# Kernel optimization log

Hardware: AMD Instinct MI355X
Metric: run time of the kernel (lower is better)

Reference implementation:

```python
import jax, jax.numpy as jnp
import numpy as np

EPS = 1e-6
BN_EPS = 1e-5
STAGES = 10


def setup_inputs() -> dict:
    key = jax.random.key(0)
    ks = jax.random.split(key, 8)
    B, L, C, K, INNER = 16, 2048, 256, 64, 4096
    x = jax.random.normal(ks[0], (B, L, C), jnp.float32)
    group_tokens = jax.random.normal(ks[1], (B, K, C), jnp.float32)
    mu0 = jax.random.normal(ks[2], (1, K, C), jnp.float32) * np.sqrt(2.0 / C)
    mu0 = mu0 / (EPS + jnp.linalg.norm(mu0, axis=2, keepdims=True))
    w1 = jax.random.normal(ks[3], (INNER, C), jnp.float32) * 0.02
    b1 = jnp.zeros((INNER,), jnp.float32)
    gamma = jnp.ones((INNER,), jnp.float32)
    beta = jnp.zeros((INNER,), jnp.float32)
    bn_mean = jnp.zeros((INNER,), jnp.float32)
    bn_var = jnp.ones((INNER,), jnp.float32)
    w2 = jax.random.normal(ks[4], (C, INNER), jnp.float32) * 0.02
    b2 = jnp.zeros((C,), jnp.float32)
    return {"x": x, "group_tokens": group_tokens, "mu0": mu0, "w1": w1,
            "b1": b1, "gamma": gamma, "beta": beta, "bn_mean": bn_mean,
            "bn_var": bn_var, "w2": w2, "b2": b2}


def _em_loop(x, mu):
    # x: [B,L,C], mu: [B,K,C]; 10-step soft-clustering fixed point (no_grad in torch)
    def step(carry, _):
        mu, _ = carry
        z = jax.nn.softmax(jnp.einsum('blc,bkc->blk', x, mu), axis=-1)  # [B,L,K]
        z = z / (EPS + z.sum(axis=1, keepdims=True))
        mu = jnp.einsum('blk,blc->bkc', z, x)
        mu = mu / (EPS + jnp.linalg.norm(mu, axis=2, keepdims=True))
        return (mu, z), None
    z0 = jnp.zeros(x.shape[:2] + (mu.shape[1],), x.dtype)
    (mu, z), _ = jax.lax.scan(step, (mu, z0), None, length=STAGES)
    return jax.lax.stop_gradient(mu), jax.lax.stop_gradient(z)


def _project_mlp(x, w1, b1, gamma, beta, bn_mean, bn_var, w2, b2):
    # Conv1d(k=1) == channelwise linear; BN in eval mode with running stats
    h = jnp.einsum('blc,ic->bli', x, w1) + b1                 # [B,L,INNER]
    h = (h - bn_mean) * (gamma / jnp.sqrt(bn_var + BN_EPS)) + beta
    h = jax.nn.relu(h)
    return jnp.einsum('bli,oi->blo', h, w2) + b2              # [B,L,C]


def reference(x, group_tokens, mu0, w1, b1, gamma, beta, bn_mean, bn_var, w2, b2):
    B = group_tokens.shape[0]
    mu = jnp.broadcast_to(mu0, (B,) + mu0.shape[1:])
    mu, z = _em_loop(x, mu)
    recon_x = jnp.einsum('blk,bkc->blc', z, mu)
    recon_x = _project_mlp(recon_x, w1, b1, gamma, beta, bn_mean, bn_var, w2, b2)
    new_z = jax.nn.softmax(jnp.einsum('blc,bkc->blk', x, mu), axis=-1)
    attn_map = new_z / (EPS + new_z.sum(axis=1, keepdims=True))  # [B,L,K]
    attn_map = jnp.transpose(attn_map, (0, 2, 1))[:, None]       # [B,1,K,L]
    return mu, attn_map, recon_x
```

## Files before the change

kernel.cpp:

```cpp
#include <hip/hip_runtime.h>

constexpr int B_ = 16, L_ = 2048, C_ = 256, K_ = 64, INNER_ = 4096;
constexpr int NCH = 16;
constexpr int RPB = 128;
#define EPSF 1e-6f

typedef __attribute__((ext_vector_type(8)))  short bf16x8;
typedef __attribute__((ext_vector_type(4)))  float f32x4;
typedef __attribute__((ext_vector_type(16))) float f32x16;
typedef _Float16 f16;
typedef __attribute__((ext_vector_type(8))) _Float16 f16x8;
typedef __attribute__((ext_vector_type(4))) _Float16 f16x4;

__device__ __forceinline__ unsigned short f2bf(float f) {
  union { float f; unsigned u; } v; v.f = f;
  unsigned r = v.u + 0x7fffu + ((v.u >> 16) & 1u);
  return (unsigned short)(r >> 16);
}

__device__ __forceinline__ void gload16(const void* src, void* lds) {
  __builtin_amdgcn_global_load_lds(
      (const __attribute__((address_space(1))) unsigned*)src,
      (__attribute__((address_space(3))) unsigned*)lds, 16, 0, 0);
}

__global__ __launch_bounds__(256) void k_prext(
    const float* __restrict__ x,
    const float* __restrict__ w1, const float* __restrict__ w2,
    const float* __restrict__ gamma, const float* __restrict__ beta,
    const float* __restrict__ bmean, const float* __restrict__ bvar,
    const float* __restrict__ b1, const float* __restrict__ mu0,
    unsigned short* __restrict__ w1fr, unsigned short* __restrict__ w2fr,
    f16* __restrict__ bnshH, f16* __restrict__ muF,
    f16* __restrict__ xf, f16* __restrict__ xTf)
{
  __shared__ float ts[64][65];
  int bid = blockIdx.x, t = threadIdx.x;
  if (bid < 4096) {
    int i = bid * 256 + t;
    if (i < INNER_ * C_) {
      int j = i & 7, l31 = (i >> 3) & 31;
      {
        int l5 = (i >> 8) & 1, ks = (i >> 9) & 15, ih = (i >> 13) & 1, ic = i >> 14;
        int r1 = ic * 64 + ih * 32 + l31;
        int c1 = ks * 16 + 4 * l5 + 8 * (j >> 2) + (j & 3);
        float sc = gamma[r1] * rsqrtf(bvar[r1] + 1e-5f);
        w1fr[i] = f2bf(w1[(size_t)r1 * C_ + c1] * sc);
      }
      {
        int ot = (i >> 8) & 7, l5 = (i >> 11) & 1, g = i >> 12;
        int o = ot * 32 + l31;
        int ii = g * 16 + 4 * l5 + 8 * (j >> 2) + (j & 3);
        w2fr[i] = f2bf(w2[(size_t)o * INNER_ + ii]);
      }
    }
    if (i < B_ * K_ * C_) muF[i] = (f16)mu0[i & (K_ * C_ - 1)];
    if (i < INNER_) {
      float sc = gamma[i] * rsqrtf(bvar[i] + 1e-5f);
      bnshH[i] = (f16)fmaf(b1[i] - bmean[i], sc, beta[i]);
    }
  } else {
    int b2 = bid - 4096;
    int l0 = (b2 & 31) * 64, c0 = ((b2 >> 5) & 3) * 64, b = b2 >> 7;
    for (int p = 0; p < 16; ++p) {
      int e = t + p * 256, i = e >> 6, j = e & 63;
      float vv = x[((size_t)b * L_ + l0 + i) * C_ + c0 + j];
      ts[i][j] = vv;
      xf[((size_t)b * L_ + l0 + i) * C_ + c0 + j] = (f16)vv;
    }
    __syncthreads();
    for (int p = 0; p < 16; ++p) {
      int e = t + p * 256, i = e >> 6, j = e & 63;
      xTf[((size_t)b * C_ + c0 + i) * L_ + l0 + j] = (f16)ts[j][i];
    }
  }
}

template<bool DO_MU, bool WRITE_Z>
__global__ __launch_bounds__(512, 2) void k_em(
    const f16* __restrict__ xf,
    const f16* __restrict__ xTf,
    const f16* __restrict__ muF,
    f16* __restrict__ zout,
    float* __restrict__ cp,
    f16* __restrict__ part)
{
  __shared__ f16 mu_s[K_ * C_];
  __shared__ f16 zT_s[K_ * RPB];
  __shared__ f16 xtile[C_ * RPB];
  __shared__ float cpart[8][K_];

  int t = threadIdx.x, b = blockIdx.y, chn = blockIdx.x, l0 = chn * RPB;
  int w = t >> 6, lane = t & 63, l15 = lane & 15, g = lane >> 4;

#pragma unroll
  for (int q = 0; q < 4; ++q) {
    int s = q * 512 + t, k = s >> 5, sl = s & 31;
    gload16(muF + (size_t)b * (K_ * C_) + k * C_ + ((sl ^ (k & 15)) << 3), mu_s + s * 8);
  }
  __builtin_amdgcn_sched_barrier(0);
  f16x8 xfr[8];
  const f16* xr = xf + ((size_t)b * L_ + l0 + w * 16 + l15) * C_ + g * 8;
#pragma unroll
  for (int ck = 0; ck < 8; ++ck) xfr[ck] = *(const f16x8*)(xr + ck * 32);
  __builtin_amdgcn_sched_barrier(0);
  if (DO_MU) {
#pragma unroll
    for (int q = 0; q < 8; ++q) {
      int s = q * 512 + t, c = s >> 4, sl = s & 15;
      gload16(xTf + (size_t)(b * C_ + c) * L_ + l0 + ((sl ^ (c & 7)) << 3), xtile + s * 8);
    }
    __builtin_amdgcn_sched_barrier(0);
    asm volatile("s_waitcnt vmcnt(16)" ::: "memory");
  } else {
    asm volatile("s_waitcnt vmcnt(8)" ::: "memory");
  }
  __builtin_amdgcn_s_barrier();
  __builtin_amdgcn_sched_barrier(0);

  f32x4 acc[4];
#pragma unroll
  for (int mt = 0; mt < 4; ++mt)
#pragma unroll
    for (int j = 0; j < 4; ++j) acc[mt][j] = 0.f;
#pragma unroll
  for (int ck = 0; ck < 8; ++ck) {
#pragma unroll
    for (int mt = 0; mt < 4; ++mt) {
      f16x8 a = *(const f16x8*)(mu_s + (mt * 16 + l15) * C_ + (((ck * 4 + g) ^ l15) << 3));
      acc[mt] = __builtin_amdgcn_mfma_f32_16x16x32_f16(a, xfr[ck], acc[mt], 0, 0, 0);
    }
  }

  float z[4][4];
  {
    float mx = acc[0][0];
#pragma unroll
    for (int mt = 0; mt < 4; ++mt)
#pragma unroll
      for (int jj = 0; jj < 4; ++jj) mx = fmaxf(mx, acc[mt][jj]);
    mx = fmaxf(mx, __shfl_xor(mx, 16, 64));
    mx = fmaxf(mx, __shfl_xor(mx, 32, 64));
    float sm = 0.f;
#pragma unroll
    for (int mt = 0; mt < 4; ++mt)
#pragma unroll
      for (int jj = 0; jj < 4; ++jj) {
        float e = __expf(acc[mt][jj] - mx);
        z[mt][jj] = e; sm += e;
      }
    sm += __shfl_xor(sm, 16, 64);
    sm += __shfl_xor(sm, 32, 64);
    float inv = 1.f / sm;
#pragma unroll
    for (int mt = 0; mt < 4; ++mt)
#pragma unroll
      for (int jj = 0; jj < 4; ++jj) z[mt][jj] *= inv;
  }

#pragma unroll
  for (int mt = 0; mt < 4; ++mt)
#pragma unroll
    for (int jj = 0; jj < 4; ++jj) {
      float v = z[mt][jj];
      v += __shfl_xor(v, 1, 64); v += __shfl_xor(v, 2, 64);
      v += __shfl_xor(v, 4, 64); v += __shfl_xor(v, 8, 64);
      if (l15 == 0) cpart[w][mt * 16 + g * 4 + jj] = v;
    }

#pragma unroll
  for (int mt = 0; mt < 4; ++mt)
#pragma unroll
    for (int jj = 0; jj < 4; ++jj) {
      int k = mt * 16 + g * 4 + jj;
      int tl = w * 16 + l15;
      f16 h = (f16)z[mt][jj];
      if (DO_MU)   zT_s[k * RPB + (((tl >> 3) ^ (k & 15)) << 3) + (tl & 7)] = h;
      if (WRITE_Z) zout[((size_t)b * L_ + l0 + tl) * K_ + k] = h;
    }
  __syncthreads();

  if (t < K_) {
    float s = 0.f;
#pragma unroll
    for (int q = 0; q < 8; ++q) s += cpart[q][t];
    cp[(size_t)chn * (B_ * K_) + b * K_ + t] = s;
  }

  if (DO_MU) {
    f32x4 a3[4][2];
#pragma unroll
    for (int mt = 0; mt < 4; ++mt)
#pragma unroll
      for (int nt = 0; nt < 2; ++nt)
#pragma unroll
        for (int j = 0; j < 4; ++j) a3[mt][nt][j] = 0.f;
    int cb = w * 32;
#pragma unroll
    for (int ks = 0; ks < 4; ++ks) {
      f16x8 az[4], bx[2];
#pragma unroll
      for (int mt = 0; mt < 4; ++mt)
        az[mt] = *(const f16x8*)(zT_s + (mt * 16 + l15) * RPB + (((ks * 4 + g) ^ l15) << 3));
#pragma unroll
      for (int nt = 0; nt < 2; ++nt) {
        int c = cb + nt * 16 + l15;
        bx[nt] = *(const f16x8*)(xtile + c * RPB + (((ks * 4 + g) ^ (c & 7)) << 3));
      }
#pragma unroll
      for (int mt = 0; mt < 4; ++mt)
#pragma unroll
        for (int nt = 0; nt < 2; ++nt)
          a3[mt][nt] = __builtin_amdgcn_mfma_f32_16x16x32_f16(az[mt], bx[nt], a3[mt][nt], 0, 0, 0);
    }
    f16* pp = part + (((size_t)chn * B_ + b) * K_) * C_;
#pragma unroll
    for (int mt = 0; mt < 4; ++mt)
#pragma unroll
      for (int nt = 0; nt < 2; ++nt)
#pragma unroll
        for (int jj = 0; jj < 4; ++jj)
          pp[(size_t)(mt * 16 + g * 4 + jj) * C_ + cb + nt * 16 + l15] = (f16)a3[mt][nt][jj];
  }
}

template<bool LAST>
__global__ __launch_bounds__(256) void k_mufin(
    const f16* __restrict__ part, const float* __restrict__ cp,
    f16* __restrict__ muF, f16* __restrict__ muT,
    float* __restrict__ zsA, float* __restrict__ outmu)
{
  int b = blockIdx.x >> 4, kg = blockIdx.x & 15, t = threadIdx.x;
  int kr = t >> 6, c4 = t & 63, k = kg * 4 + kr;
  float a0 = 0.f, a1 = 0.f, a2 = 0.f, a3 = 0.f;
#pragma unroll
  for (int chn = 0; chn < NCH; ++chn) {
    f16x4 p = *(const f16x4*)(part + (((size_t)chn * B_ + b) * K_ + k) * C_ + c4 * 4);
    a0 += (float)p[0]; a1 += (float)p[1]; a2 += (float)p[2]; a3 += (float)p[3];
  }
  float zs = 0.f;
#pragma unroll
  for (int chn = 0; chn < NCH; ++chn) zs += cp[(size_t)chn * (B_ * K_) + b * K_ + k];
  float sc = 1.f / (EPSF + zs);
  a0 *= sc; a1 *= sc; a2 *= sc; a3 *= sc;
  float ssq = a0 * a0 + a1 * a1 + a2 * a2 + a3 * a3;
#pragma unroll
  for (int off = 32; off >= 1; off >>= 1) ssq += __shfl_xor(ssq, off, 64);
  float inv = 1.f / (EPSF + sqrtf(ssq));
  a0 *= inv; a1 *= inv; a2 *= inv; a3 *= inv;
  size_t base = (size_t)(b * K_ + k) * C_ + c4 * 4;
  f16x4 hm; hm[0] = (f16)a0; hm[1] = (f16)a1; hm[2] = (f16)a2; hm[3] = (f16)a3;
  *(f16x4*)(muF + base) = hm;
  if (c4 == 0) zsA[b * K_ + k] = zs;
  if (LAST) {
    *(float4*)(outmu + base) = make_float4(a0, a1, a2, a3);
    muT[((size_t)b * C_ + c4 * 4 + 0) * K_ + k] = hm[0];
    muT[((size_t)b * C_ + c4 * 4 + 1) * K_ + k] = hm[1];
    muT[((size_t)b * C_ + c4 * 4 + 2) * K_ + k] = hm[2];
    muT[((size_t)b * C_ + c4 * 4 + 3) * K_ + k] = hm[3];
  }
}

__global__ __launch_bounds__(256) void k_attn(
    const f16* __restrict__ zB, const float* __restrict__ cpB, float* __restrict__ attn)
{
  __shared__ float zt[64][68];
  __shared__ float inv_s[K_];
  int b = blockIdx.y, l0 = blockIdx.x * 64, t = threadIdx.x;
  if (t < K_) {
    float zs = 0.f;
#pragma unroll
    for (int chn = 0; chn < NCH; ++chn) zs += cpB[(size_t)chn * (B_ * K_) + b * K_ + t];
    inv_s[t] = 1.f / (EPSF + zs);
  }
  for (int p = 0; p < 16; ++p) {
    int e = t + p * 256, lo = e >> 6, k = e & 63;
    zt[lo][k] = (float)zB[((size_t)b * L_ + l0 + lo) * K_ + k];
  }
  __syncthreads();
  int lo = t & 63, kb = t >> 6;
  for (int p = 0; p < 16; ++p) {
    int k = kb * 16 + p;
    attn[((size_t)b * K_ + k) * L_ + l0 + lo] = zt[lo][k] * inv_s[k];
  }
}

constexpr int W1S_OFF  = 0;
constexpr int W2S_OFF  = 65536;
constexpr int BNS_OFF  = 131072;
constexpr int ZINV_OFF = 139264;
constexpr int POOL_SZ  = 139520;

__global__ __launch_bounds__(512, 2) void k_mlp(
    const f16* __restrict__ zA,
    const f16* __restrict__ muT,
    const float* __restrict__ zsA,
    const unsigned short* __restrict__ w1fr,
    const unsigned short* __restrict__ w2fr,
    const f16* __restrict__ bnshH, const float* __restrict__ b2,
    float* __restrict__ outr)
{
  __shared__ __align__(16) char pool[POOL_SZ];
  unsigned short* w1s = (unsigned short*)(pool + W1S_OFF);
  unsigned short* w2s = (unsigned short*)(pool + W2S_OFF);
  f16* bns_s          = (f16*)(pool + BNS_OFF);
  float* zinv_s       = (float*)(pool + ZINV_OFF);
  f16* muT_s          = (f16*)(pool + W1S_OFF + 32768);
  f16* z_s            = (f16*)(pool + W2S_OFF + 32768);

  int t = threadIdx.x, w = t >> 6, lane = t & 63, l31 = lane & 31, l5 = lane >> 5;
  int rb = blockIdx.x * 128, b = rb >> 11, l0 = rb & 2047;
  int tt = w & 3, ih = w >> 2;

#define STAGE(ic, buf)                                                    \
  {                                                                       \
    _Pragma("unroll")                                                     \
    for (int q = 0; q < 4; ++q) {                                         \
      int d2 = q * 512 + t;                                               \
      gload16(w1fr + (size_t)(ic) * 16384 + d2 * 8,                       \
              w1s + (size_t)(buf) * 16384 + d2 * 8);                      \
    }                                                                     \
    _Pragma("unroll")                                                     \
    for (int q = 0; q < 4; ++q) {                                         \
      int d2 = q * 512 + t;                                               \
      gload16(w2fr + (size_t)(ic) * 16384 + d2 * 8,                       \
              w2s + (size_t)(buf) * 16384 + d2 * 8);                      \
    }                                                                     \
  }

  if (t < K_) zinv_s[t] = 1.f / (EPSF + zsA[b * K_ + t]);
  __builtin_amdgcn_sched_barrier(0);
#pragma unroll
  for (int q = 0; q < 4; ++q) {
    int s = q * 512 + t, c = s >> 3, sl = s & 7;
    gload16(muT + ((size_t)b * C_ + c) * K_ + ((sl ^ (c & 7)) << 3), muT_s + s * 8);
  }
#pragma unroll
  for (int q = 0; q < 2; ++q) {
    int s = q * 512 + t, tok = s >> 3, sl = s & 7;
    gload16(zA + ((size_t)b * L_ + l0 + tok) * K_ + ((sl ^ (tok & 7)) << 3), z_s + s * 8);
  }
  gload16(bnshH + t * 8, bns_s + t * 8);
  __builtin_amdgcn_sched_barrier(0);
  STAGE(0, 0);
  __builtin_amdgcn_sched_barrier(0);
  asm volatile("s_waitcnt vmcnt(8) lgkmcnt(0)" ::: "memory");
  __builtin_amdgcn_s_barrier();
  __builtin_amdgcn_sched_barrier(0);

  bf16x8 rc[16];
  {
    f16x8 bz[4];
#pragma unroll
    for (int kk = 0; kk < 4; ++kk) {
      int tok = tt * 32 + l31;
      f16x8 zr = *(const f16x8*)(z_s + tok * 64 + (((kk * 2 + l5) ^ (tok & 7)) << 3));
      f16x8 sc2;
#pragma unroll
      for (int e = 0; e < 8; ++e)
        sc2[e] = (f16)((float)zr[e] * zinv_s[kk * 16 + l5 * 8 + e]);
      bz[kk] = sc2;
    }
    f32x16 d[8];
#pragma unroll
    for (int m = 0; m < 8; ++m)
#pragma unroll
      for (int r = 0; r < 16; ++r) d[m][r] = 0.f;
#pragma unroll
    for (int kk = 0; kk < 4; ++kk) {
#pragma unroll
      for (int m = 0; m < 8; ++m) {
        int c = m * 32 + l31;
        f16x8 am = *(const f16x8*)(muT_s + c * 64 + (((kk * 2 + l5) ^ (c & 7)) << 3));
        d[m] = __builtin_amdgcn_mfma_f32_32x32x16_f16(am, bz[kk], d[m], 0, 0, 0);
      }
    }
    union Uf { unsigned u[4]; bf16x8 v; } rcU[16];
#pragma unroll
    for (int m = 0; m < 8; ++m)
#pragma unroll
      for (int q = 0; q < 8; ++q) {
        unsigned u = (unsigned)f2bf(d[m][2 * q]) | ((unsigned)f2bf(d[m][2 * q + 1]) << 16);
        rcU[2 * m + (q >> 2)].u[q & 3] = u;
      }
#pragma unroll
    for (int ks = 0; ks < 16; ++ks) rc[ks] = rcU[ks].v;
  }
  asm volatile("s_waitcnt lgkmcnt(0)" ::: "memory");
  __builtin_amdgcn_s_barrier();
  __builtin_amdgcn_sched_barrier(0);

  f32x16 acc2[8];
#pragma unroll
  for (int ot = 0; ot < 8; ++ot)
#pragma unroll
    for (int r = 0; r < 16; ++r) acc2[ot][r] = 0.f;

  const unsigned short* p1base = w1s + ih * 8192 + l5 * 256 + l31 * 8;
  const unsigned short* p2base = w2s + ih * 8192 + l5 * 2048 + l31 * 8;

  for (int ic = 0; ic < 64; ++ic) {
    int cur = ic & 1;
    asm volatile("s_waitcnt vmcnt(0)" ::: "memory");
    __builtin_amdgcn_s_barrier();
    __builtin_amdgcn_sched_barrier(0);
    if (ic < 63) STAGE(ic + 1, cur ^ 1);
    __builtin_amdgcn_sched_barrier(0);

    f32x16 h0, h1;
#pragma unroll
    for (int r = 0; r < 16; ++r) { h0[r] = 0.f; h1[r] = 0.f; }
    const unsigned short* p1 = p1base + cur * 16384;
    __builtin_amdgcn_s_setprio(1);
#pragma unroll
    for (int ks = 0; ks < 16; ++ks) {
      bf16x8 a1 = *(const bf16x8*)(p1 + ks * 512);
      if (ks & 1) h1 = __builtin_amdgcn_mfma_f32_32x32x16_bf16(a1, rc[ks], h1, 0, 0, 0);
      else        h0 = __builtin_amdgcn_mfma_f32_32x32x16_bf16(a1, rc[ks], h0, 0, 0, 0);
    }
    __builtin_amdgcn_s_setprio(0);
#pragma unroll
    for (int r = 0; r < 16; ++r) h0[r] += h1[r];

    f16x4 bnv[4];
#pragma unroll
    for (int q = 0; q < 4; ++q)
      bnv[q] = *(const f16x4*)(bns_s + ic * 64 + ih * 32 + 8 * q + 4 * l5);
    unsigned pk[8];
#pragma unroll
    for (int q = 0; q < 4; ++q) {
#pragma unroll
      for (int pr = 0; pr < 2; ++pr) {
        int r0 = q * 4 + pr * 2;
        float v0 = fmaxf(h0[r0]     + (float)bnv[q][pr * 2],     0.f);
        float v1 = fmaxf(h0[r0 + 1] + (float)bnv[q][pr * 2 + 1], 0.f);
        pk[q * 2 + pr] = (unsigned)f2bf(v0) | ((unsigned)f2bf(v1) << 16);
      }
    }
    union Uf { unsigned u[4]; bf16x8 v; };
    Uf bfr0, bfr1;
#pragma unroll
    for (int m = 0; m < 4; ++m) { bfr0.u[m] = pk[m]; bfr1.u[m] = pk[4 + m]; }

    const unsigned short* p2 = p2base + cur * 16384;
    __builtin_amdgcn_s_setprio(1);
#pragma unroll
    for (int s = 0; s < 2; ++s) {
      bf16x8 bfv = s ? bfr1.v : bfr0.v;
#pragma unroll
      for (int ot = 0; ot < 8; ++ot) {
        bf16x8 a2 = *(const bf16x8*)(p2 + s * 4096 + ot * 256);
        acc2[ot] = __builtin_amdgcn_mfma_f32_32x32x16_bf16(a2, bfv, acc2[ot], 0, 0, 0);
      }
    }
    __builtin_amdgcn_s_setprio(0);
  }
#undef STAGE

  __syncthreads();
  float* red = (float*)pool;
  if (ih == 1) {
#pragma unroll
    for (int ot = 0; ot < 8; ++ot)
#pragma unroll
      for (int r = 0; r < 16; ++r)
        red[((tt * 8 + ot) * 16 + r) * 64 + lane] = acc2[ot][r];
  }
  __syncthreads();
  if (ih == 0) {
    int tok = rb + tt * 32 + l31;
#pragma unroll
    for (int ot = 0; ot < 8; ++ot) {
#pragma unroll
      for (int r = 0; r < 16; ++r)
        acc2[ot][r] += red[((tt * 8 + ot) * 16 + r) * 64 + lane];
#pragma unroll
      for (int q = 0; q < 4; ++q) {
        int o = ot * 32 + 8 * q + 4 * l5;
        float4 bias = *(const float4*)(b2 + o);
        f32x4 v;
        v[0] = acc2[ot][q * 4 + 0] + bias.x;
        v[1] = acc2[ot][q * 4 + 1] + bias.y;
        v[2] = acc2[ot][q * 4 + 2] + bias.z;
        v[3] = acc2[ot][q * 4 + 3] + bias.w;
        *(f32x4*)(outr + (size_t)tok * C_ + o) = v;
      }
    }
  }
}

extern "C" void kernel_launch(void* const* d_in, const int* in_sizes, int n_in,
                              void* d_out, int out_size, void* d_ws, size_t ws_size,
                              hipStream_t stream)
{
  const float* x     = (const float*)d_in[0];
  const float* mu0   = (const float*)d_in[2];
  const float* w1    = (const float*)d_in[3];
  const float* b1    = (const float*)d_in[4];
  const float* gamma = (const float*)d_in[5];
  const float* beta  = (const float*)d_in[6];
  const float* bmean = (const float*)d_in[7];
  const float* bvar  = (const float*)d_in[8];
  const float* w2    = (const float*)d_in[9];
  const float* b2    = (const float*)d_in[10];
  float* out = (float*)d_out;

  char* wsb = (char*)d_ws;
  f16* part = (f16*)(wsb + 0);
  f16* zB   = part;
  f16* zA   = (f16*)(wsb + 8388608);
  f16* xf   = (f16*)(wsb + 12582912);
  f16* xTf  = (f16*)(wsb + 29360128);
  unsigned short* w1fr = (unsigned short*)(wsb + 46137344);
  unsigned short* w2fr = (unsigned short*)(wsb + 48234496);
  f16*   muF   = (f16*)(wsb + 50331648);
  f16*   muT   = (f16*)(wsb + 50855936);
  f16*   bnshH = (f16*)(wsb + 51380224);
  float* cpA   = (float*)(wsb + 51388416);
  float* cpB   = (float*)(wsb + 51453952);
  float* zsA   = (float*)(wsb + 51519488);

  k_prext<<<6144, 256, 0, stream>>>(x, w1, w2, gamma, beta, bmean, bvar, b1, mu0,
                                    w1fr, w2fr, bnshH, muF, xf, xTf);

  for (int s = 0; s < 10; ++s) {
    if (s == 9) k_em<true, true ><<<dim3(NCH, 16), 512, 0, stream>>>(xf, xTf, muF, zA, cpA, part);
    else        k_em<true, false><<<dim3(NCH, 16), 512, 0, stream>>>(xf, xTf, muF, zA, cpA, part);
    if (s == 9) k_mufin<true ><<<256, 256, 0, stream>>>(part, cpA, muF, muT, zsA, out);
    else        k_mufin<false><<<256, 256, 0, stream>>>(part, cpA, muF, muT, zsA, out);
  }
  k_em<false, true><<<dim3(NCH, 16), 512, 0, stream>>>(xf, xTf, muF, zB, cpB, part);
  k_attn<<<dim3(32, 16), 256, 0, stream>>>(zB, cpB, out + 262144);
  k_mlp<<<256, 512, 0, stream>>>(zA, muT, zsA, w1fr, w2fr, bnshH, b2, out + 2359296);
}
```

Baseline: 323.2 us.

## Halve MLP block to 64 tokens and single-buffer weight staging

The MLP kernel now runs 512 blocks of 256 threads, each covering 64 tokens instead of 128, and drops the double-buffered LDS weight staging. LDS use roughly halves, so more blocks can be resident per CU and the grid fills the GPU more evenly. The next chunk's weights are now loaded only after the current chunk's MFMAs finish, followed by a full wait at the top of each iteration. This exposes global-load latency on every iteration, and the smaller token tile means each weight chunk is reused across fewer tokens, so total weight traffic doubles.

```diff
diff --git a/kernel.cpp b/kernel.cpp
--- a/kernel.cpp
+++ b/kernel.cpp
@@ -286,12 +286,12 @@
 }
 
 constexpr int W1S_OFF  = 0;
-constexpr int W2S_OFF  = 65536;
-constexpr int BNS_OFF  = 131072;
-constexpr int ZINV_OFF = 139264;
-constexpr int POOL_SZ  = 139520;
-
-__global__ __launch_bounds__(512, 2) void k_mlp(
+constexpr int W2S_OFF  = 32768;
+constexpr int BNS_OFF  = 65536;
+constexpr int ZINV_OFF = 73728;
+constexpr int POOL_SZ  = 73984;
+
+__global__ __launch_bounds__(256, 2) void k_mlp(
     const f16* __restrict__ zA,
     const f16* __restrict__ muT,
     const float* __restrict__ zsA,
@@ -305,46 +305,45 @@
   unsigned short* w2s = (unsigned short*)(pool + W2S_OFF);
   f16* bns_s          = (f16*)(pool + BNS_OFF);
   float* zinv_s       = (float*)(pool + ZINV_OFF);
-  f16* muT_s          = (f16*)(pool + W1S_OFF + 32768);
-  f16* z_s            = (f16*)(pool + W2S_OFF + 32768);
+  f16* muT_s          = (f16*)(pool + W1S_OFF);
+  f16* z_s            = (f16*)(pool + W2S_OFF);
 
   int t = threadIdx.x, w = t >> 6, lane = t & 63, l31 = lane & 31, l5 = lane >> 5;
-  int rb = blockIdx.x * 128, b = rb >> 11, l0 = rb & 2047;
-  int tt = w & 3, ih = w >> 2;
-
-#define STAGE(ic, buf)                                                    \
+  int rb = blockIdx.x * 64, b = rb >> 11, l0 = rb & 2047;
+  int tt = w & 1, ih = w >> 1;
+
+#define STAGE(ic)                                                         \
   {                                                                       \
     _Pragma("unroll")                                                     \
-    for (int q = 0; q < 4; ++q) {                                         \
-      int d2 = q * 512 + t;                                               \
-      gload16(w1fr + (size_t)(ic) * 16384 + d2 * 8,                       \
-              w1s + (size_t)(buf) * 16384 + d2 * 8);                      \
+    for (int q = 0; q < 8; ++q) {                                         \
+      int d2 = q * 256 + t;                                               \
+      gload16(w1fr + (size_t)(ic) * 16384 + d2 * 8, w1s + d2 * 8);        \
     }                                                                     \
     _Pragma("unroll")                                                     \
-    for (int q = 0; q < 4; ++q) {                                         \
-      int d2 = q * 512 + t;                                               \
-      gload16(w2fr + (size_t)(ic) * 16384 + d2 * 8,                       \
-              w2s + (size_t)(buf) * 16384 + d2 * 8);                      \
+    for (int q = 0; q < 8; ++q) {                                         \
+      int d2 = q * 256 + t;                                               \
+      gload16(w2fr + (size_t)(ic) * 16384 + d2 * 8, w2s + d2 * 8);        \
     }                                                                     \
   }
 
   if (t < K_) zinv_s[t] = 1.f / (EPSF + zsA[b * K_ + t]);
   __builtin_amdgcn_sched_barrier(0);
 #pragma unroll
-  for (int q = 0; q < 4; ++q) {
-    int s = q * 512 + t, c = s >> 3, sl = s & 7;
+  for (int q = 0; q < 8; ++q) {
+    int s = q * 256 + t, c = s >> 3, sl = s & 7;
     gload16(muT + ((size_t)b * C_ + c) * K_ + ((sl ^ (c & 7)) << 3), muT_s + s * 8);
   }
 #pragma unroll
   for (int q = 0; q < 2; ++q) {
-    int s = q * 512 + t, tok = s >> 3, sl = s & 7;
+    int s = q * 256 + t, tok = s >> 3, sl = s & 7;
     gload16(zA + ((size_t)b * L_ + l0 + tok) * K_ + ((sl ^ (tok & 7)) << 3), z_s + s * 8);
   }
-  gload16(bnshH + t * 8, bns_s + t * 8);
-  __builtin_amdgcn_sched_barrier(0);
-  STAGE(0, 0);
-  __builtin_amdgcn_sched_barrier(0);
-  asm volatile("s_waitcnt vmcnt(8) lgkmcnt(0)" ::: "memory");
+#pragma unroll
+  for (int q = 0; q < 2; ++q) {
+    int s = q * 256 + t;
+    gload16(bnshH + s * 8, bns_s + s * 8);
+  }
+  asm volatile("s_waitcnt vmcnt(0) lgkmcnt(0)" ::: "memory");
   __builtin_amdgcn_s_barrier();
   __builtin_amdgcn_sched_barrier(0);
 
@@ -396,25 +395,22 @@
 #pragma unroll
     for (int r = 0; r < 16; ++r) acc2[ot][r] = 0.f;
 
+  STAGE(0);
   const unsigned short* p1base = w1s + ih * 8192 + l5 * 256 + l31 * 8;
   const unsigned short* p2base = w2s + ih * 8192 + l5 * 2048 + l31 * 8;
 
   for (int ic = 0; ic < 64; ++ic) {
-    int cur = ic & 1;
     asm volatile("s_waitcnt vmcnt(0)" ::: "memory");
     __builtin_amdgcn_s_barrier();
     __builtin_amdgcn_sched_barrier(0);
-    if (ic < 63) STAGE(ic + 1, cur ^ 1);
-    __builtin_amdgcn_sched_barrier(0);
 
     f32x16 h0, h1;
 #pragma unroll
     for (int r = 0; r < 16; ++r) { h0[r] = 0.f; h1[r] = 0.f; }
-    const unsigned short* p1 = p1base + cur * 16384;
     __builtin_amdgcn_s_setprio(1);
 #pragma unroll
     for (int ks = 0; ks < 16; ++ks) {
-      bf16x8 a1 = *(const bf16x8*)(p1 + ks * 512);
+      bf16x8 a1 = *(const bf16x8*)(p1base + ks * 512);
       if (ks & 1) h1 = __builtin_amdgcn_mfma_f32_32x32x16_bf16(a1, rc[ks], h1, 0, 0, 0);
       else        h0 = __builtin_amdgcn_mfma_f32_32x32x16_bf16(a1, rc[ks], h0, 0, 0, 0);
     }
@@ -442,18 +438,23 @@
 #pragma unroll
     for (int m = 0; m < 4; ++m) { bfr0.u[m] = pk[m]; bfr1.u[m] = pk[4 + m]; }
 
-    const unsigned short* p2 = p2base + cur * 16384;
     __builtin_amdgcn_s_setprio(1);
 #pragma unroll
     for (int s = 0; s < 2; ++s) {
       bf16x8 bfv = s ? bfr1.v : bfr0.v;
 #pragma unroll
       for (int ot = 0; ot < 8; ++ot) {
-        bf16x8 a2 = *(const bf16x8*)(p2 + s * 4096 + ot * 256);
+        bf16x8 a2 = *(const bf16x8*)(p2base + s * 4096 + ot * 256);
         acc2[ot] = __builtin_amdgcn_mfma_f32_32x32x16_bf16(a2, bfv, acc2[ot], 0, 0, 0);
       }
     }
     __builtin_amdgcn_s_setprio(0);
+
+    asm volatile("s_waitcnt lgkmcnt(0)" ::: "memory");
+    __builtin_amdgcn_s_barrier();
+    __builtin_amdgcn_sched_barrier(0);
+    if (ic < 63) STAGE(ic + 1);
+    __builtin_amdgcn_sched_barrier(0);
   }
 #undef STAGE
 
@@ -531,5 +532,5 @@
   }
   k_em<false, true><<<dim3(NCH, 16), 512, 0, stream>>>(xf, xTf, muF, zB, cpB, part);
   k_attn<<<dim3(32, 16), 256, 0, stream>>>(zB, cpB, out + 262144);
-  k_mlp<<<256, 512, 0, stream>>>(zA, muT, zsA, w1fr, w2fr, bnshH, b2, out + 2359296);
-}
+  k_mlp<<<512, 256, 0, stream>>>(zA, muT, zsA, w1fr, w2fr, bnshH, b2, out + 2359296);
+}
```

Measured after the change: 338.2 us. 1.05x slower.
